# Kernel optimization log

Measured on AMD Instinct MI355X. Metric: run time of the kernel, lower is better.

## Reference

```python
import jax, jax.numpy as jnp
import numpy as np

N_ITEMS = 1_000_000
EMBED_DIM = 4
N_EDGES = 10_000_000


def setup_inputs() -> dict:
    key = jax.random.key(0)
    kx, ke_i, ke_j, kw = jax.random.split(key, 4)
    X = jax.random.normal(kx, (N_ITEMS, EMBED_DIM), dtype=jnp.float32)
    i = jax.random.randint(ke_i, (N_EDGES,), 0, N_ITEMS, dtype=jnp.int64)
    j = jax.random.randint(ke_j, (N_EDGES,), 0, N_ITEMS, dtype=jnp.int64)
    # MDE forbids self edges; bump j where it collides with i
    j = jnp.where(i == j, (j + 1) % N_ITEMS, j)
    edges = jnp.stack([i, j], axis=1)  # [p, 2] int64
    weights = jax.random.uniform(kw, (N_EDGES,), dtype=jnp.float32)
    return {"X": X, "edges": edges, "weights": weights}


def reference(X, edges, weights):
    # differences: X[i] - X[j] per edge (gather -> subtract)  [p, m]
    diff = X[edges[:, 0]] - X[edges[:, 1]]
    # distances: per-edge L2 norm  [p]
    dist = jnp.sqrt(jnp.sum(diff * diff, axis=1))
    # distortion function (quadratic penalty): w_k * d_k^2  [p]
    distortions = weights * dist * dist
    # average distortion (scalar)
    return jnp.mean(distortions)
```

## Files before the change

kernel.cpp:

```cpp
#include <hip/hip_runtime.h>
#include <hip/hip_bf16.h>


typedef float f32x2 __attribute__((ext_vector_type(2)));
typedef float f32x4 __attribute__((ext_vector_type(4)));
typedef int   i32x4 __attribute__((ext_vector_type(4)));

__device__ __forceinline__ i32x4 make_rsrc(const void* p, unsigned int bytes) {
    i32x4 r;
    unsigned long long up = (unsigned long long)p;
    r.x = (int)(up & 0xFFFFFFFFull);
    r.y = (int)(up >> 32);
    r.z = (int)bytes;
    r.w = 0x00020000;
    return r;
}

#define GATHER_SC0(dst, rsrc, idx)                                       \
    asm volatile("buffer_load_dword %0, %1, %2, 0 offen sc0"             \
                 : "=v"(dst) : "v"((idx) << 2), "s"(rsrc))

__global__ __launch_bounds__(256) void x_to_fp8_kernel(
    const float4* __restrict__ X4,
    unsigned int* __restrict__ rows,
    int n_items)
{
    int idx    = blockIdx.x * blockDim.x + threadIdx.x;
    int stride = gridDim.x * blockDim.x;
    for (int k = idx; k < n_items; k += stride) {
        float4 a = X4[k];
        int p = __builtin_amdgcn_cvt_pk_fp8_f32(a.x, a.y, 0, false);
        p     = __builtin_amdgcn_cvt_pk_fp8_f32(a.z, a.w, p, true);
        rows[k] = (unsigned int)p;
    }
}

__device__ __forceinline__ float edge_term(unsigned int ra, unsigned int rb, float wk) {
    f32x2 alo = __builtin_amdgcn_cvt_pk_f32_fp8(ra, false);
    f32x2 ahi = __builtin_amdgcn_cvt_pk_f32_fp8(ra, true);
    f32x2 blo = __builtin_amdgcn_cvt_pk_f32_fp8(rb, false);
    f32x2 bhi = __builtin_amdgcn_cvt_pk_f32_fp8(rb, true);
    float d0 = alo.x - blo.x;
    float d1 = alo.y - blo.y;
    float d2 = ahi.x - bhi.x;
    float d3 = ahi.y - bhi.y;
    return wk * (d0 * d0 + d1 * d1 + d2 * d2 + d3 * d3);
}

__global__ __launch_bounds__(256) void mde_fp8_l2_kernel(
    const unsigned int* __restrict__ rows,
    const i32x4*        __restrict__ edges4,
    const f32x4*        __restrict__ w4,
    float*              __restrict__ out,
    int n_items,
    int n_batches,
    int n_edges_tail_start, int n_edges, float inv_n,
    const int*   __restrict__ edges_flat,
    const float* __restrict__ w_flat)
{
    float acc0 = 0.0f, acc1 = 0.0f;
    int tid    = blockIdx.x * blockDim.x + threadIdx.x;
    int stride = gridDim.x * blockDim.x;

    i32x4 rsrc = make_rsrc(rows, (unsigned int)n_items * 4u);

    for (int b = tid; b < n_batches; b += stride) {
        i32x4 e0 = __builtin_nontemporal_load(&edges4[b * 4 + 0]);
        i32x4 e1 = __builtin_nontemporal_load(&edges4[b * 4 + 1]);
        i32x4 e2 = __builtin_nontemporal_load(&edges4[b * 4 + 2]);
        i32x4 e3 = __builtin_nontemporal_load(&edges4[b * 4 + 3]);
        f32x4 wa = __builtin_nontemporal_load(&w4[b * 2 + 0]);
        f32x4 wb = __builtin_nontemporal_load(&w4[b * 2 + 1]);

        unsigned int r0a, r0b, r1a, r1b, r2a, r2b, r3a, r3b;
        unsigned int r4a, r4b, r5a, r5b, r6a, r6b, r7a, r7b;
        GATHER_SC0(r0a, rsrc, e0.x); GATHER_SC0(r0b, rsrc, e0.y);
        GATHER_SC0(r1a, rsrc, e0.z); GATHER_SC0(r1b, rsrc, e0.w);
        GATHER_SC0(r2a, rsrc, e1.x); GATHER_SC0(r2b, rsrc, e1.y);
        GATHER_SC0(r3a, rsrc, e1.z); GATHER_SC0(r3b, rsrc, e1.w);
        GATHER_SC0(r4a, rsrc, e2.x); GATHER_SC0(r4b, rsrc, e2.y);
        GATHER_SC0(r5a, rsrc, e2.z); GATHER_SC0(r5b, rsrc, e2.w);
        GATHER_SC0(r6a, rsrc, e3.x); GATHER_SC0(r6b, rsrc, e3.y);
        GATHER_SC0(r7a, rsrc, e3.z); GATHER_SC0(r7b, rsrc, e3.w);

        asm volatile("s_waitcnt vmcnt(0)" ::: "memory");
        __builtin_amdgcn_sched_barrier(0);

        acc0 += edge_term(r0a, r0b, wa.x);
        acc1 += edge_term(r1a, r1b, wa.y);
        acc0 += edge_term(r2a, r2b, wa.z);
        acc1 += edge_term(r3a, r3b, wa.w);
        acc0 += edge_term(r4a, r4b, wb.x);
        acc1 += edge_term(r5a, r5b, wb.y);
        acc0 += edge_term(r6a, r6b, wb.z);
        acc1 += edge_term(r7a, r7b, wb.w);
    }

    for (int k = n_edges_tail_start + tid; k < n_edges; k += stride) {
        int ei = edges_flat[2 * k];
        int ej = edges_flat[2 * k + 1];
        acc0 += edge_term(rows[ei], rows[ej], w_flat[k]);
    }

    float acc = acc0 + acc1;

    #pragma unroll
    for (int off = 32; off > 0; off >>= 1)
        acc += __shfl_down(acc, off, 64);

    __shared__ float smem[4];
    int lane = threadIdx.x & 63;
    int wave = threadIdx.x >> 6;
    if (lane == 0) smem[wave] = acc;
    __syncthreads();

    if (threadIdx.x == 0) {
        float s = smem[0] + smem[1] + smem[2] + smem[3];
        atomicAdd(out, s * inv_n);
    }
}

__global__ __launch_bounds__(256) void mde_distortion_kernel(
    const float4* __restrict__ X4,
    const int2*   __restrict__ edges,
    const float*  __restrict__ w,
    float*        __restrict__ out,
    int n_edges, float inv_n)
{
    float acc = 0.0f;
    int tid    = blockIdx.x * blockDim.x + threadIdx.x;
    int stride = gridDim.x * blockDim.x;
    for (int k = tid; k < n_edges; k += stride) {
        int2   e = edges[k];
        float4 a = X4[e.x];
        float4 b = X4[e.y];
        float dx = a.x - b.x, dy = a.y - b.y, dz = a.z - b.z, dw = a.w - b.w;
        acc += w[k] * (dx * dx + dy * dy + dz * dz + dw * dw);
    }
    #pragma unroll
    for (int off = 32; off > 0; off >>= 1)
        acc += __shfl_down(acc, off, 64);
    __shared__ float smem[4];
    int lane = threadIdx.x & 63;
    int wave = threadIdx.x >> 6;
    if (lane == 0) smem[wave] = acc;
    __syncthreads();
    if (threadIdx.x == 0) {
        float s = smem[0] + smem[1] + smem[2] + smem[3];
        atomicAdd(out, s * inv_n);
    }
}

extern "C" void kernel_launch(void* const* d_in, const int* in_sizes, int n_in,
                              void* d_out, int out_size, void* d_ws, size_t ws_size,
                              hipStream_t stream) {
    const float* X     = (const float*)d_in[0];
    const int*   edges = (const int*)d_in[1];
    const float* w     = (const float*)d_in[2];
    float* out = (float*)d_out;

    int n_edges = in_sizes[2];
    int n_items = in_sizes[0] / 4;
    float inv_n = (float)(1.0 / (double)n_edges);

    (void)hipMemsetAsync(out, 0, sizeof(float), stream);

    const int block = 256;
    size_t need = (size_t)n_items * sizeof(unsigned int);

    if (ws_size >= need) {
        unsigned int* rows = (unsigned int*)d_ws;
        int grid_prep = (n_items + block - 1) / block;
        x_to_fp8_kernel<<<grid_prep, block, 0, stream>>>(
            (const float4*)X, rows, n_items);

        int n_batches = n_edges / 8;
        int tail_start = n_batches * 8;
        mde_fp8_l2_kernel<<<4096, block, 0, stream>>>(
            rows, (const i32x4*)edges, (const f32x4*)w, out,
            n_items, n_batches, tail_start, n_edges, inv_n, edges, w);
    } else {
        mde_distortion_kernel<<<4096, block, 0, stream>>>(
            (const float4*)X, (const int2*)edges, w, out, n_edges, inv_n);
    }
}
```

Baseline: 246.7 us.

## Software-pipeline fp8 gather kernel over three fixed batches with buffer loads

Replaces the grid-stride loop with a fully unrolled kernel where each thread handles exactly three batches of eight edges. All edge and weight streams are issued up front as non-temporal buffer loads, and each batch's row gathers are issued while the previous batch's terms are computed. Grid drops to 2048 blocks with a 4-waves occupancy hint. Out-of-range batches rely on buffer bounds checks returning zero. The fast path only applies when the edge count fits in three passes of the grid, so it is tuned to this problem size and higher register use may lower occupancy.

After: 254.3 us. 3.1% more time.

```diff
diff --git a/kernel.cpp b/kernel.cpp
--- a/kernel.cpp
+++ b/kernel.cpp
@@ -16,9 +16,17 @@
     return r;
 }
 
-#define GATHER_SC0(dst, rsrc, idx)                                       \
+#define GATHER_SC0(dst, rsrc, voff)                                      \
     asm volatile("buffer_load_dword %0, %1, %2, 0 offen sc0"             \
-                 : "=v"(dst) : "v"((idx) << 2), "s"(rsrc))
+                 : "=v"(dst) : "v"(voff), "s"(rsrc))
+
+#define STREAM_X4(dst, rsrc, voff)                                       \
+    asm volatile("buffer_load_dwordx4 %0, %1, %2, 0 offen nt"            \
+                 : "=v"(dst) : "v"(voff), "s"(rsrc))
+
+#define WAITCNT(n)                                                       \
+    do { asm volatile("s_waitcnt vmcnt(" #n ")" ::: "memory");           \
+         __builtin_amdgcn_sched_barrier(0); } while (0)
 
 __global__ __launch_bounds__(256) void x_to_fp8_kernel(
     const float4* __restrict__ X4,
@@ -47,59 +55,101 @@
     return wk * (d0 * d0 + d1 * d1 + d2 * d2 + d3 * d3);
 }
 
-__global__ __launch_bounds__(256) void mde_fp8_l2_kernel(
+#define ISSUE_GATHERS(e0, e1, e2, e3)                                    \
+    GATHER_SC0(g0a, rsR, e0.x << 2); GATHER_SC0(g0b, rsR, e0.y << 2);    \
+    GATHER_SC0(g1a, rsR, e0.z << 2); GATHER_SC0(g1b, rsR, e0.w << 2);    \
+    GATHER_SC0(g2a, rsR, e1.x << 2); GATHER_SC0(g2b, rsR, e1.y << 2);    \
+    GATHER_SC0(g3a, rsR, e1.z << 2); GATHER_SC0(g3b, rsR, e1.w << 2);    \
+    GATHER_SC0(g4a, rsR, e2.x << 2); GATHER_SC0(g4b, rsR, e2.y << 2);    \
+    GATHER_SC0(g5a, rsR, e2.z << 2); GATHER_SC0(g5b, rsR, e2.w << 2);    \
+    GATHER_SC0(g6a, rsR, e3.x << 2); GATHER_SC0(g6b, rsR, e3.y << 2);    \
+    GATHER_SC0(g7a, rsR, e3.z << 2); GATHER_SC0(g7b, rsR, e3.w << 2)
+
+#define ACCUM_TERMS(wa, wb)                                              \
+    acc0 += edge_term(g0a, g0b, wa.x);                                   \
+    acc1 += edge_term(g1a, g1b, wa.y);                                   \
+    acc0 += edge_term(g2a, g2b, wa.z);                                   \
+    acc1 += edge_term(g3a, g3b, wa.w);                                   \
+    acc0 += edge_term(g4a, g4b, wb.x);                                   \
+    acc1 += edge_term(g5a, g5b, wb.y);                                   \
+    acc0 += edge_term(g6a, g6b, wb.z);                                   \
+    acc1 += edge_term(g7a, g7b, wb.w)
+
+__global__ __launch_bounds__(256, 4) void mde_fp8_pipe_kernel(
     const unsigned int* __restrict__ rows,
-    const i32x4*        __restrict__ edges4,
-    const f32x4*        __restrict__ w4,
+    const int*          __restrict__ edges,
+    const float*        __restrict__ w,
     float*              __restrict__ out,
     int n_items,
     int n_batches,
-    int n_edges_tail_start, int n_edges, float inv_n,
-    const int*   __restrict__ edges_flat,
-    const float* __restrict__ w_flat)
+    int n_edges_tail_start, int n_edges, float inv_n)
 {
     float acc0 = 0.0f, acc1 = 0.0f;
-    int tid    = blockIdx.x * blockDim.x + threadIdx.x;
-    int stride = gridDim.x * blockDim.x;
-
-    i32x4 rsrc = make_rsrc(rows, (unsigned int)n_items * 4u);
-
-    for (int b = tid; b < n_batches; b += stride) {
-        i32x4 e0 = __builtin_nontemporal_load(&edges4[b * 4 + 0]);
-        i32x4 e1 = __builtin_nontemporal_load(&edges4[b * 4 + 1]);
-        i32x4 e2 = __builtin_nontemporal_load(&edges4[b * 4 + 2]);
-        i32x4 e3 = __builtin_nontemporal_load(&edges4[b * 4 + 3]);
-        f32x4 wa = __builtin_nontemporal_load(&w4[b * 2 + 0]);
-        f32x4 wb = __builtin_nontemporal_load(&w4[b * 2 + 1]);
-
-        unsigned int r0a, r0b, r1a, r1b, r2a, r2b, r3a, r3b;
-        unsigned int r4a, r4b, r5a, r5b, r6a, r6b, r7a, r7b;
-        GATHER_SC0(r0a, rsrc, e0.x); GATHER_SC0(r0b, rsrc, e0.y);
-        GATHER_SC0(r1a, rsrc, e0.z); GATHER_SC0(r1b, rsrc, e0.w);
-        GATHER_SC0(r2a, rsrc, e1.x); GATHER_SC0(r2b, rsrc, e1.y);
-        GATHER_SC0(r3a, rsrc, e1.z); GATHER_SC0(r3b, rsrc, e1.w);
-        GATHER_SC0(r4a, rsrc, e2.x); GATHER_SC0(r4b, rsrc, e2.y);
-        GATHER_SC0(r5a, rsrc, e2.z); GATHER_SC0(r5b, rsrc, e2.w);
-        GATHER_SC0(r6a, rsrc, e3.x); GATHER_SC0(r6b, rsrc, e3.y);
-        GATHER_SC0(r7a, rsrc, e3.z); GATHER_SC0(r7b, rsrc, e3.w);
-
-        asm volatile("s_waitcnt vmcnt(0)" ::: "memory");
-        __builtin_amdgcn_sched_barrier(0);
-
-        acc0 += edge_term(r0a, r0b, wa.x);
-        acc1 += edge_term(r1a, r1b, wa.y);
-        acc0 += edge_term(r2a, r2b, wa.z);
-        acc1 += edge_term(r3a, r3b, wa.w);
-        acc0 += edge_term(r4a, r4b, wb.x);
-        acc1 += edge_term(r5a, r5b, wb.y);
-        acc0 += edge_term(r6a, r6b, wb.z);
-        acc1 += edge_term(r7a, r7b, wb.w);
-    }
-
-    for (int k = n_edges_tail_start + tid; k < n_edges; k += stride) {
-        int ei = edges_flat[2 * k];
-        int ej = edges_flat[2 * k + 1];
-        acc0 += edge_term(rows[ei], rows[ej], w_flat[k]);
+    int tid = blockIdx.x * blockDim.x + threadIdx.x;
+    int T   = gridDim.x * blockDim.x;
+
+    i32x4 rsR = make_rsrc(rows,  (unsigned int)n_items * 4u);
+    i32x4 rsE = make_rsrc(edges, (unsigned int)n_batches * 64u);
+    i32x4 rsW = make_rsrc(w,     (unsigned int)n_batches * 32u);
+
+    int bA = tid, bB = tid + T, bC = tid + 2 * T;
+
+    i32x4 eA0, eA1, eA2, eA3, eB0, eB1, eB2, eB3, eC0, eC1, eC2, eC3;
+    f32x4 wA0, wA1, wB0, wB1, wC0, wC1;
+    STREAM_X4(eA0, rsE, bA * 64 +  0); STREAM_X4(eA1, rsE, bA * 64 + 16);
+    STREAM_X4(eA2, rsE, bA * 64 + 32); STREAM_X4(eA3, rsE, bA * 64 + 48);
+    STREAM_X4(wA0, rsW, bA * 32 +  0); STREAM_X4(wA1, rsW, bA * 32 + 16);
+    STREAM_X4(eB0, rsE, bB * 64 +  0); STREAM_X4(eB1, rsE, bB * 64 + 16);
+    STREAM_X4(eB2, rsE, bB * 64 + 32); STREAM_X4(eB3, rsE, bB * 64 + 48);
+    STREAM_X4(wB0, rsW, bB * 32 +  0); STREAM_X4(wB1, rsW, bB * 32 + 16);
+    STREAM_X4(eC0, rsE, bC * 64 +  0); STREAM_X4(eC1, rsE, bC * 64 + 16);
+    STREAM_X4(eC2, rsE, bC * 64 + 32); STREAM_X4(eC3, rsE, bC * 64 + 48);
+    STREAM_X4(wC0, rsW, bC * 32 +  0); STREAM_X4(wC1, rsW, bC * 32 + 16);
+
+    unsigned int g0a, g0b, g1a, g1b, g2a, g2b, g3a, g3b;
+    unsigned int g4a, g4b, g5a, g5b, g6a, g6b, g7a, g7b;
+
+    WAITCNT(12);
+    ISSUE_GATHERS(eA0, eA1, eA2, eA3);
+    WAITCNT(0);
+    {
+        unsigned int h0a = g0a, h0b = g0b, h1a = g1a, h1b = g1b;
+        unsigned int h2a = g2a, h2b = g2b, h3a = g3a, h3b = g3b;
+        unsigned int h4a = g4a, h4b = g4b, h5a = g5a, h5b = g5b;
+        unsigned int h6a = g6a, h6b = g6b, h7a = g7a, h7b = g7b;
+        ISSUE_GATHERS(eB0, eB1, eB2, eB3);
+        acc0 += edge_term(h0a, h0b, wA0.x);
+        acc1 += edge_term(h1a, h1b, wA0.y);
+        acc0 += edge_term(h2a, h2b, wA0.z);
+        acc1 += edge_term(h3a, h3b, wA0.w);
+        acc0 += edge_term(h4a, h4b, wA1.x);
+        acc1 += edge_term(h5a, h5b, wA1.y);
+        acc0 += edge_term(h6a, h6b, wA1.z);
+        acc1 += edge_term(h7a, h7b, wA1.w);
+    }
+    WAITCNT(0);
+    {
+        unsigned int h0a = g0a, h0b = g0b, h1a = g1a, h1b = g1b;
+        unsigned int h2a = g2a, h2b = g2b, h3a = g3a, h3b = g3b;
+        unsigned int h4a = g4a, h4b = g4b, h5a = g5a, h5b = g5b;
+        unsigned int h6a = g6a, h6b = g6b, h7a = g7a, h7b = g7b;
+        ISSUE_GATHERS(eC0, eC1, eC2, eC3);
+        acc0 += edge_term(h0a, h0b, wB0.x);
+        acc1 += edge_term(h1a, h1b, wB0.y);
+        acc0 += edge_term(h2a, h2b, wB0.z);
+        acc1 += edge_term(h3a, h3b, wB0.w);
+        acc0 += edge_term(h4a, h4b, wB1.x);
+        acc1 += edge_term(h5a, h5b, wB1.y);
+        acc0 += edge_term(h6a, h6b, wB1.z);
+        acc1 += edge_term(h7a, h7b, wB1.w);
+    }
+    WAITCNT(0);
+    ACCUM_TERMS(wC0, wC1);
+
+    for (int k = n_edges_tail_start + tid; k < n_edges; k += T) {
+        int ei = edges[2 * k];
+        int ej = edges[2 * k + 1];
+        acc0 += edge_term(rows[ei], rows[ej], w[k]);
     }
 
     float acc = acc0 + acc1;
@@ -166,19 +216,22 @@
     (void)hipMemsetAsync(out, 0, sizeof(float), stream);
 
     const int block = 256;
+    const int grid  = 2048;
+    long long T = (long long)grid * block;
     size_t need = (size_t)n_items * sizeof(unsigned int);
 
-    if (ws_size >= need) {
+    int n_batches = n_edges / 8;
+    int tail_start = n_batches * 8;
+
+    if (ws_size >= need && (long long)n_batches <= 3 * T) {
         unsigned int* rows = (unsigned int*)d_ws;
         int grid_prep = (n_items + block - 1) / block;
         x_to_fp8_kernel<<<grid_prep, block, 0, stream>>>(
             (const float4*)X, rows, n_items);
 
-        int n_batches = n_edges / 8;
-        int tail_start = n_batches * 8;
-        mde_fp8_l2_kernel<<<4096, block, 0, stream>>>(
-            rows, (const i32x4*)edges, (const f32x4*)w, out,
-            n_items, n_batches, tail_start, n_edges, inv_n, edges, w);
+        mde_fp8_pipe_kernel<<<grid, block, 0, stream>>>(
+            rows, edges, w, out,
+            n_items, n_batches, tail_start, n_edges, inv_n);
     } else {
         mde_distortion_kernel<<<4096, block, 0, stream>>>(
             (const float4*)X, (const int2*)edges, w, out, n_edges, inv_n);
```
